# Kernel optimization log

Hardware: AMD Instinct MI355X
Metric: run time of the kernel (lower is better)

Reference implementation:

```python
import jax, jax.numpy as jnp
import numpy as np

H = 32  # hidden size (hard-coded in the torch module)

def _lstm_layer(x, W_ih, W_hh):
    # x: [B, T, F]; W_ih: [4H, F]; W_hh: [4H, H]; bias=False
    B = x.shape[0]
    # precompute input projection for all timesteps: [T, B, 4H]
    xg = jnp.einsum('btf,gf->tbg', x, W_ih)
    WhhT = W_hh.T  # [H, 4H]
    def step(carry, xg_t):
        h, c = carry
        gates = xg_t + h @ WhhT          # [B, 4H]
        i, f, g, o = jnp.split(gates, 4, axis=-1)  # PyTorch gate order i,f,g,o
        i = jax.nn.sigmoid(i)
        f = jax.nn.sigmoid(f)
        g = jnp.tanh(g)
        o = jax.nn.sigmoid(o)
        c = f * c + i * g
        h = o * jnp.tanh(c)
        return (h, c), h
    h0 = jnp.zeros((B, H), x.dtype)
    c0 = jnp.zeros((B, H), x.dtype)
    (hT, cT), hs = jax.lax.scan(step, (h0, c0), xg)
    return jnp.transpose(hs, (1, 0, 2)), hT, cT  # outputs [B,T,H], final h, final c


def setup_inputs() -> dict:
    key = jax.random.key(0)
    ks = jax.random.split(key, 8)
    B, T, F = 8192, 60, 158
    s_in = 1.0 / np.sqrt(H)  # PyTorch LSTM init scale
    inp = {
        'x':     jax.random.normal(ks[0], (B, T, F), jnp.float32),
        'W_ih0': jax.random.uniform(ks[1], (4 * H, F), jnp.float32, -s_in, s_in),
        'W_hh0': jax.random.uniform(ks[2], (4 * H, H), jnp.float32, -s_in, s_in),
        'W_ih1': jax.random.uniform(ks[3], (4 * H, H), jnp.float32, -s_in, s_in),
        'W_hh1': jax.random.uniform(ks[4], (4 * H, H), jnp.float32, -s_in, s_in),
        'W1':    jax.random.uniform(ks[5], (16, H), jnp.float32, -s_in, s_in),
        'b1':    jax.random.uniform(ks[6], (16,), jnp.float32, -s_in, s_in),
        'W2':    jax.random.uniform(ks[7], (1, 16), jnp.float32, -0.25, 0.25),
    }
    return inp


def reference(x, W_ih0, W_hh0, W_ih1, W_hh1, W1, b1, W2):
    out1, h1, c1 = _lstm_layer(x, W_ih0, W_hh0)      # layer 1 (inter-layer dropout inactive at eval)
    out2, h2, c2 = _lstm_layer(out1, W_ih1, W_hh1)   # layer 2
    # torch code: output, h_n = lstm(x) -> h_n is the TUPLE (h_n, c_n),
    # so h_n[-1] == c_n with shape [num_layers=2, B, H]
    c_n = jnp.stack([c1, c2], axis=0)                 # [2, B, H]
    y = jax.nn.relu(c_n @ W1.T + b1) @ W2.T           # [2, B, 1]
    return y
```

## Files before the change

### kernel.cpp

```cpp
#include <hip/hip_runtime.h>


constexpr int Bn = 8192, Tn = 60, Fn = 158, Hn = 32, Gn = 128;
constexpr int SKX = 168;
constexpr int SKH = 40;

typedef __attribute__((ext_vector_type(8))) short short8;
typedef __attribute__((ext_vector_type(4))) float floatx4;

__device__ __forceinline__ float sigm_(float x) {
    return __fdividef(1.f, 1.f + __expf(-x));
}
__device__ __forceinline__ float tanh_(float x) {
    return 1.f - __fdividef(2.f, __expf(2.f * x) + 1.f);
}
__device__ __forceinline__ unsigned short bf16r(float x) {
    unsigned u = __float_as_uint(x);
    return (unsigned short)((u + 0x7fffu + ((u >> 16) & 1u)) >> 16);
}
__device__ __forceinline__ float bf16f(unsigned short h) {
    return __uint_as_float(((unsigned)h) << 16);
}
__device__ __forceinline__ void cvt8(const float* v, short8& hi, short8& lo) {
#pragma unroll
    for (int j = 0; j < 8; ++j) {
        unsigned short h = bf16r(v[j]);
        hi[j] = (short)h;
        lo[j] = (short)bf16r(v[j] - bf16f(h));
    }
}

__global__ __launch_bounds__(256, 2) void lstm2_fused_kernel(
    const float* __restrict__ x,
    const float* __restrict__ Wih0, const float* __restrict__ Whh0,
    const float* __restrict__ Wih1, const float* __restrict__ Whh1,
    const float* __restrict__ W1, const float* __restrict__ b1,
    const float* __restrict__ W2, float* __restrict__ out) {
    __shared__ unsigned short sXh[2 * 16 * SKX];
    __shared__ unsigned short sXl[2 * 16 * SKX];
    __shared__ unsigned short sH1h[16 * SKH], sH1l[16 * SKH];
    __shared__ unsigned short sH2h[16 * SKH], sH2l[16 * SKH];
    __shared__ float sG[16 * 132];

    const int tid = threadIdx.x;
    const int wave = tid >> 6, lane = tid & 63;
    const int quad = lane >> 4, l15 = lane & 15;
    const int bBase = blockIdx.x * 16;

    short8 bX[5][2][2];
#pragma unroll
    for (int nt = 0; nt < 2; ++nt) {
        const int n = wave * 32 + nt * 16 + l15;
#pragma unroll
        for (int ks = 0; ks < 5; ++ks) {
            float wv[8];
#pragma unroll
            for (int j = 0; j < 8; ++j) {
                int k = ks * 32 + quad * 8 + j;
                wv[j] = (k < Fn) ? Wih0[n * Fn + k] : 0.f;
            }
            cvt8(wv, bX[ks][nt][0], bX[ks][nt][1]);
        }
    }
    short8 bW[3][2][2];
    const float* Wp[3] = {Whh0, Wih1, Whh1};
#pragma unroll
    for (int m = 0; m < 3; ++m)
#pragma unroll
        for (int nt = 0; nt < 2; ++nt) {
            const int n = wave * 32 + nt * 16 + l15;
            const float* wp = Wp[m] + n * Hn + quad * 8;
            float4 q0 = *(const float4*)(wp);
            float4 q1 = *(const float4*)(wp + 4);
            float wv[8] = {q0.x, q0.y, q0.z, q0.w, q1.x, q1.y, q1.z, q1.w};
            cvt8(wv, bW[m][nt][0], bW[m][nt][1]);
        }

    const float* xp[5];
    int soff[5];
    bool act[5];
#pragma unroll
    for (int r = 0; r < 5; ++r) {
        int i = tid + r * 256;
        act[r] = (i < 1264);
        int row = i / 79, c = i - row * 79;
        if (!act[r]) { row = 0; c = 0; }
        soff[r] = row * (SKX / 2) + c;
        xp[r] = x + (size_t)(bBase + row) * (Tn * Fn) + 2 * c;
    }
    auto stage = [&](const float2* v, int buf) {
        unsigned* dh = (unsigned*)sXh + buf * (16 * SKX / 2);
        unsigned* dl = (unsigned*)sXl + buf * (16 * SKX / 2);
#pragma unroll
        for (int r = 0; r < 5; ++r) {
            if (act[r]) {
                unsigned short h0 = bf16r(v[r].x), h1 = bf16r(v[r].y);
                unsigned short l0 = bf16r(v[r].x - bf16f(h0));
                unsigned short l1 = bf16r(v[r].y - bf16f(h1));
                dh[soff[r]] = (unsigned)h0 | ((unsigned)h1 << 16);
                dl[soff[r]] = (unsigned)l0 | ((unsigned)l1 << 16);
            }
        }
    };

    for (int i = tid; i < 320; i += 256) {
        ((unsigned*)sH1h)[i] = 0; ((unsigned*)sH1l)[i] = 0;
        ((unsigned*)sH2h)[i] = 0; ((unsigned*)sH2l)[i] = 0;
    }
    if (tid < 32) {
        int buf = tid >> 4, row = tid & 15;
        ((unsigned*)sXh)[buf * 1344 + row * 84 + 79] = 0;
        ((unsigned*)sXl)[buf * 1344 + row * 84 + 79] = 0;
    }

    {
        float2 v[5];
#pragma unroll
        for (int r = 0; r < 5; ++r) {
            v[r] = act[r] ? *(const float2*)xp[r] : make_float2(0.f, 0.f);
            xp[r] += Fn;
        }
        stage(v, 0);
    }

    const int aOffH = l15 * SKH + quad * 8;
    const int urow = tid >> 4, uj = (tid & 15) * 2;
    float c1x = 0.f, c1y = 0.f, c2x = 0.f, c2y = 0.f;
    __syncthreads();

    for (int t = 0; t < Tn; ++t) {
        const int buf = t & 1;
        float2 xr[5];
        if (t < Tn - 1) {
#pragma unroll
            for (int r = 0; r < 5; ++r) {
                xr[r] = act[r] ? *(const float2*)xp[r] : make_float2(0.f, 0.f);
                xp[r] += Fn;
            }
        }

        {
            const unsigned short* bxh = sXh + buf * (16 * SKX);
            const unsigned short* bxl = sXl + buf * (16 * SKX);
            short8 a1h = *(const short8*)(sH1h + aOffH);
            short8 a1l = *(const short8*)(sH1l + aOffH);
            floatx4 acc[2] = {};
#pragma unroll
            for (int ks = 0; ks < 5; ++ks) {
                const int off = l15 * SKX + ks * 32 + quad * 8;
                short8 xh = *(const short8*)(bxh + off);
                short8 xl = *(const short8*)(bxl + off);
#pragma unroll
                for (int nt = 0; nt < 2; ++nt) {
                    acc[nt] = __builtin_amdgcn_mfma_f32_16x16x32_bf16(xh, bX[ks][nt][0], acc[nt], 0, 0, 0);
                    acc[nt] = __builtin_amdgcn_mfma_f32_16x16x32_bf16(xh, bX[ks][nt][1], acc[nt], 0, 0, 0);
                    acc[nt] = __builtin_amdgcn_mfma_f32_16x16x32_bf16(xl, bX[ks][nt][0], acc[nt], 0, 0, 0);
                }
            }
#pragma unroll
            for (int nt = 0; nt < 2; ++nt) {
                acc[nt] = __builtin_amdgcn_mfma_f32_16x16x32_bf16(a1h, bW[0][nt][0], acc[nt], 0, 0, 0);
                acc[nt] = __builtin_amdgcn_mfma_f32_16x16x32_bf16(a1h, bW[0][nt][1], acc[nt], 0, 0, 0);
                acc[nt] = __builtin_amdgcn_mfma_f32_16x16x32_bf16(a1l, bW[0][nt][0], acc[nt], 0, 0, 0);
            }
#pragma unroll
            for (int nt = 0; nt < 2; ++nt)
#pragma unroll
                for (int reg = 0; reg < 4; ++reg)
                    sG[(quad * 4 + reg) * 132 + wave * 32 + nt * 16 + l15] = acc[nt][reg];
        }
        __syncthreads();

        {
            const float* g0 = sG + urow * 132 + uj;
            float2 ig = *(const float2*)(g0);
            float2 fg = *(const float2*)(g0 + 32);
            float2 gg = *(const float2*)(g0 + 64);
            float2 og = *(const float2*)(g0 + 96);
            c1x = sigm_(fg.x) * c1x + sigm_(ig.x) * tanh_(gg.x);
            c1y = sigm_(fg.y) * c1y + sigm_(ig.y) * tanh_(gg.y);
            float h0 = sigm_(og.x) * tanh_(c1x);
            float h1v = sigm_(og.y) * tanh_(c1y);
            unsigned short h0h = bf16r(h0), h1h = bf16r(h1v);
            unsigned short h0l = bf16r(h0 - bf16f(h0h)), h1l = bf16r(h1v - bf16f(h1h));
            *(unsigned*)(sH1h + urow * SKH + uj) = (unsigned)h0h | ((unsigned)h1h << 16);
            *(unsigned*)(sH1l + urow * SKH + uj) = (unsigned)h0l | ((unsigned)h1l << 16);
        }
        __syncthreads();

        {
            short8 a1h = *(const short8*)(sH1h + aOffH);
            short8 a1l = *(const short8*)(sH1l + aOffH);
            short8 a2h = *(const short8*)(sH2h + aOffH);
            short8 a2l = *(const short8*)(sH2l + aOffH);
            floatx4 acc[2] = {};
#pragma unroll
            for (int nt = 0; nt < 2; ++nt) {
                acc[nt] = __builtin_amdgcn_mfma_f32_16x16x32_bf16(a1h, bW[1][nt][0], acc[nt], 0, 0, 0);
                acc[nt] = __builtin_amdgcn_mfma_f32_16x16x32_bf16(a1h, bW[1][nt][1], acc[nt], 0, 0, 0);
                acc[nt] = __builtin_amdgcn_mfma_f32_16x16x32_bf16(a1l, bW[1][nt][0], acc[nt], 0, 0, 0);
                acc[nt] = __builtin_amdgcn_mfma_f32_16x16x32_bf16(a2h, bW[2][nt][0], acc[nt], 0, 0, 0);
                acc[nt] = __builtin_amdgcn_mfma_f32_16x16x32_bf16(a2h, bW[2][nt][1], acc[nt], 0, 0, 0);
                acc[nt] = __builtin_amdgcn_mfma_f32_16x16x32_bf16(a2l, bW[2][nt][0], acc[nt], 0, 0, 0);
            }
#pragma unroll
            for (int nt = 0; nt < 2; ++nt)
#pragma unroll
                for (int reg = 0; reg < 4; ++reg)
                    sG[(quad * 4 + reg) * 132 + wave * 32 + nt * 16 + l15] = acc[nt][reg];
        }
        if (t < Tn - 1) stage(xr, buf ^ 1);
        __syncthreads();

        {
            const float* g0 = sG + urow * 132 + uj;
            float2 ig = *(const float2*)(g0);
            float2 fg = *(const float2*)(g0 + 32);
            float2 gg = *(const float2*)(g0 + 64);
            float2 og = *(const float2*)(g0 + 96);
            c2x = sigm_(fg.x) * c2x + sigm_(ig.x) * tanh_(gg.x);
            c2y = sigm_(fg.y) * c2y + sigm_(ig.y) * tanh_(gg.y);
            float h0 = sigm_(og.x) * tanh_(c2x);
            float h1v = sigm_(og.y) * tanh_(c2y);
            unsigned short h0h = bf16r(h0), h1h = bf16r(h1v);
            unsigned short h0l = bf16r(h0 - bf16f(h0h)), h1l = bf16r(h1v - bf16f(h1h));
            *(unsigned*)(sH2h + urow * SKH + uj) = (unsigned)h0h | ((unsigned)h1h << 16);
            *(unsigned*)(sH2l + urow * SKH + uj) = (unsigned)h0l | ((unsigned)h1l << 16);
        }
        __syncthreads();
    }

    float* sC = sG;
    *(float2*)(sC + urow * 33 + uj) = make_float2(c1x, c1y);
    *(float2*)(sC + 528 + urow * 33 + uj) = make_float2(c2x, c2y);
    __syncthreads();
    if (tid < 32) {
        int l = tid >> 4, b = tid & 15;
        const float* cc = sC + l * 528 + b * 33;
        float y = 0.f;
#pragma unroll 1
        for (int q = 0; q < 16; ++q) {
            float s = b1[q];
#pragma unroll
            for (int j = 0; j < 32; ++j) s = fmaf(cc[j], W1[q * 32 + j], s);
            y = fmaf(fmaxf(s, 0.f), W2[q], y);
        }
        out[l * Bn + bBase + b] = y;
    }
}

extern "C" void kernel_launch(void* const* d_in, const int* in_sizes, int n_in,
                              void* d_out, int out_size, void* d_ws, size_t ws_size,
                              hipStream_t stream) {
    const float* x    = (const float*)d_in[0];
    const float* Wih0 = (const float*)d_in[1];
    const float* Whh0 = (const float*)d_in[2];
    const float* Wih1 = (const float*)d_in[3];
    const float* Whh1 = (const float*)d_in[4];
    const float* W1   = (const float*)d_in[5];
    const float* b1   = (const float*)d_in[6];
    const float* W2   = (const float*)d_in[7];
    float* out = (float*)d_out;

    lstm2_fused_kernel<<<Bn / 16, 256, 0, stream>>>(x, Wih0, Whh0, Wih1, Whh1,
                                                    W1, b1, W2, out);
}
```

Measured before the change: 489.4 us.

## Skew LSTM layers across timesteps, switch to fp16 split with scaled residual

```diff
diff --git a/kernel.cpp b/kernel.cpp
--- a/kernel.cpp
+++ b/kernel.cpp
@@ -1,11 +1,15 @@
 #include <hip/hip_runtime.h>
 
 
-constexpr int Bn = 8192, Tn = 60, Fn = 158, Hn = 32, Gn = 128;
+constexpr int Bn = 8192, Tn = 60, Fn = 158, Hn = 32;
 constexpr int SKX = 168;
 constexpr int SKH = 40;
-
-typedef __attribute__((ext_vector_type(8))) short short8;
+constexpr int SG = 132;
+constexpr float LS = 4096.f;
+constexpr float ILS = 1.f / 4096.f;
+
+typedef _Float16 half8 __attribute__((ext_vector_type(8)));
+typedef __fp16 half2f __attribute__((ext_vector_type(2)));
 typedef __attribute__((ext_vector_type(4))) float floatx4;
 
 __device__ __forceinline__ float sigm_(float x) {
@@ -14,19 +18,18 @@
 __device__ __forceinline__ float tanh_(float x) {
     return 1.f - __fdividef(2.f, __expf(2.f * x) + 1.f);
 }
-__device__ __forceinline__ unsigned short bf16r(float x) {
-    unsigned u = __float_as_uint(x);
-    return (unsigned short)((u + 0x7fffu + ((u >> 16) & 1u)) >> 16);
-}
-__device__ __forceinline__ float bf16f(unsigned short h) {
-    return __uint_as_float(((unsigned)h) << 16);
-}
-__device__ __forceinline__ void cvt8(const float* v, short8& hi, short8& lo) {
-#pragma unroll
-    for (int j = 0; j < 8; ++j) {
-        unsigned short h = bf16r(v[j]);
-        hi[j] = (short)h;
-        lo[j] = (short)bf16r(v[j] - bf16f(h));
+__device__ __forceinline__ unsigned h2u(half2f h) {
+    return __builtin_bit_cast(unsigned, h);
+}
+__device__ __forceinline__ void cvt8h(const float* v, half8& hi, half8& lo) {
+#pragma unroll
+    for (int j = 0; j < 8; j += 2) {
+        half2f h = __builtin_amdgcn_cvt_pkrtz(v[j], v[j + 1]);
+        float r0 = (v[j] - (float)h[0]) * LS;
+        float r1 = (v[j + 1] - (float)h[1]) * LS;
+        half2f l = __builtin_amdgcn_cvt_pkrtz(r0, r1);
+        hi[j] = (_Float16)h[0]; hi[j + 1] = (_Float16)h[1];
+        lo[j] = (_Float16)l[0]; lo[j + 1] = (_Float16)l[1];
     }
 }
 
@@ -40,14 +43,15 @@
     __shared__ unsigned short sXl[2 * 16 * SKX];
     __shared__ unsigned short sH1h[16 * SKH], sH1l[16 * SKH];
     __shared__ unsigned short sH2h[16 * SKH], sH2l[16 * SKH];
-    __shared__ float sG[16 * 132];
+    __shared__ float sG1[16 * SG];
+    __shared__ float sG2[16 * SG];
 
     const int tid = threadIdx.x;
     const int wave = tid >> 6, lane = tid & 63;
     const int quad = lane >> 4, l15 = lane & 15;
     const int bBase = blockIdx.x * 16;
 
-    short8 bX[5][2][2];
+    half8 bX[5][2][2];
 #pragma unroll
     for (int nt = 0; nt < 2; ++nt) {
         const int n = wave * 32 + nt * 16 + l15;
@@ -59,10 +63,10 @@
                 int k = ks * 32 + quad * 8 + j;
                 wv[j] = (k < Fn) ? Wih0[n * Fn + k] : 0.f;
             }
-            cvt8(wv, bX[ks][nt][0], bX[ks][nt][1]);
-        }
-    }
-    short8 bW[3][2][2];
+            cvt8h(wv, bX[ks][nt][0], bX[ks][nt][1]);
+        }
+    }
+    half8 bW[3][2][2];
     const float* Wp[3] = {Whh0, Wih1, Whh1};
 #pragma unroll
     for (int m = 0; m < 3; ++m)
@@ -73,7 +77,7 @@
             float4 q0 = *(const float4*)(wp);
             float4 q1 = *(const float4*)(wp + 4);
             float wv[8] = {q0.x, q0.y, q0.z, q0.w, q1.x, q1.y, q1.z, q1.w};
-            cvt8(wv, bW[m][nt][0], bW[m][nt][1]);
+            cvt8h(wv, bW[m][nt][0], bW[m][nt][1]);
         }
 
     const float* xp[5];
@@ -94,11 +98,11 @@
 #pragma unroll
         for (int r = 0; r < 5; ++r) {
             if (act[r]) {
-                unsigned short h0 = bf16r(v[r].x), h1 = bf16r(v[r].y);
-                unsigned short l0 = bf16r(v[r].x - bf16f(h0));
-                unsigned short l1 = bf16r(v[r].y - bf16f(h1));
-                dh[soff[r]] = (unsigned)h0 | ((unsigned)h1 << 16);
-                dl[soff[r]] = (unsigned)l0 | ((unsigned)l1 << 16);
+                half2f h = __builtin_amdgcn_cvt_pkrtz(v[r].x, v[r].y);
+                half2f l = __builtin_amdgcn_cvt_pkrtz(
+                    (v[r].x - (float)h[0]) * LS, (v[r].y - (float)h[1]) * LS);
+                dh[soff[r]] = h2u(h);
+                dl[soff[r]] = h2u(l);
             }
         }
     };
@@ -113,126 +117,156 @@
         ((unsigned*)sXl)[buf * 1344 + row * 84 + 79] = 0;
     }
 
-    {
+#pragma unroll
+    for (int t0 = 0; t0 < 2; ++t0) {
         float2 v[5];
 #pragma unroll
         for (int r = 0; r < 5; ++r) {
             v[r] = act[r] ? *(const float2*)xp[r] : make_float2(0.f, 0.f);
             xp[r] += Fn;
         }
-        stage(v, 0);
+        stage(v, t0);
     }
 
     const int aOffH = l15 * SKH + quad * 8;
-    const int urow = tid >> 4, uj = (tid & 15) * 2;
+    const int urow = tid >> 4, hp = (tid & 15) * 2;
     float c1x = 0.f, c1y = 0.f, c2x = 0.f, c2y = 0.f;
-    __syncthreads();
-
-    for (int t = 0; t < Tn; ++t) {
-        const int buf = t & 1;
+
+    auto upd = [&](const float* sGx, unsigned short* sHh, unsigned short* sHl,
+                   float& cx, float& cy) {
+        const float* g = sGx + urow * SG + hp * 4;
+        float4 A = *(const float4*)g;
+        float4 Bv = *(const float4*)(g + 4);
+        cx = sigm_(A.y) * cx + sigm_(A.x) * tanh_(A.z);
+        cy = sigm_(Bv.y) * cy + sigm_(Bv.x) * tanh_(Bv.z);
+        float h0 = sigm_(A.w) * tanh_(cx);
+        float h1v = sigm_(Bv.w) * tanh_(cy);
+        half2f hh = __builtin_amdgcn_cvt_pkrtz(h0, h1v);
+        half2f hl = __builtin_amdgcn_cvt_pkrtz((h0 - (float)hh[0]) * LS,
+                                               (h1v - (float)hh[1]) * LS);
+        *(unsigned*)(sHh + urow * SKH + hp) = h2u(hh);
+        *(unsigned*)(sHl + urow * SKH + hp) = h2u(hl);
+    };
+
+    __syncthreads();
+
+    {
+        floatx4 aH[2] = {}, aL[2] = {};
+#pragma unroll
+        for (int ks = 0; ks < 5; ++ks) {
+            const int off = l15 * SKX + ks * 32 + quad * 8;
+            half8 xh = *(const half8*)(sXh + off);
+            half8 xl = *(const half8*)(sXl + off);
+#pragma unroll
+            for (int nt = 0; nt < 2; ++nt) {
+                aH[nt] = __builtin_amdgcn_mfma_f32_16x16x32_f16(xh, bX[ks][nt][0], aH[nt], 0, 0, 0);
+                aL[nt] = __builtin_amdgcn_mfma_f32_16x16x32_f16(xh, bX[ks][nt][1], aL[nt], 0, 0, 0);
+                aL[nt] = __builtin_amdgcn_mfma_f32_16x16x32_f16(xl, bX[ks][nt][0], aL[nt], 0, 0, 0);
+            }
+        }
+#pragma unroll
+        for (int nt = 0; nt < 2; ++nt)
+#pragma unroll
+            for (int reg = 0; reg < 4; ++reg)
+                sG1[(quad * 4 + reg) * SG + (nt * 16 + l15) * 4 + wave] =
+                    fmaf(ILS, aL[nt][reg], aH[nt][reg]);
+    }
+    __syncthreads();
+    upd(sG1, sH1h, sH1l, c1x, c1y);
+    __syncthreads();
+
+    for (int i = 0; i < Tn - 1; ++i) {
         float2 xr[5];
-        if (t < Tn - 1) {
+        const bool pf = (i + 2 < Tn);
+        if (pf) {
 #pragma unroll
             for (int r = 0; r < 5; ++r) {
                 xr[r] = act[r] ? *(const float2*)xp[r] : make_float2(0.f, 0.f);
                 xp[r] += Fn;
             }
         }
-
         {
-            const unsigned short* bxh = sXh + buf * (16 * SKX);
-            const unsigned short* bxl = sXl + buf * (16 * SKX);
-            short8 a1h = *(const short8*)(sH1h + aOffH);
-            short8 a1l = *(const short8*)(sH1l + aOffH);
-            floatx4 acc[2] = {};
+            const unsigned short* bxh = sXh + ((i + 1) & 1) * (16 * SKX);
+            const unsigned short* bxl = sXl + ((i + 1) & 1) * (16 * SKX);
+            half8 a1h = *(const half8*)(sH1h + aOffH);
+            half8 a1l = *(const half8*)(sH1l + aOffH);
+            half8 a2h = *(const half8*)(sH2h + aOffH);
+            half8 a2l = *(const half8*)(sH2l + aOffH);
+            floatx4 a1H[2] = {}, a1L[2] = {}, a2H[2] = {}, a2L[2] = {};
 #pragma unroll
             for (int ks = 0; ks < 5; ++ks) {
                 const int off = l15 * SKX + ks * 32 + quad * 8;
-                short8 xh = *(const short8*)(bxh + off);
-                short8 xl = *(const short8*)(bxl + off);
+                half8 xh = *(const half8*)(bxh + off);
+                half8 xl = *(const half8*)(bxl + off);
 #pragma unroll
                 for (int nt = 0; nt < 2; ++nt) {
-                    acc[nt] = __builtin_amdgcn_mfma_f32_16x16x32_bf16(xh, bX[ks][nt][0], acc[nt], 0, 0, 0);
-                    acc[nt] = __builtin_amdgcn_mfma_f32_16x16x32_bf16(xh, bX[ks][nt][1], acc[nt], 0, 0, 0);
-                    acc[nt] = __builtin_amdgcn_mfma_f32_16x16x32_bf16(xl, bX[ks][nt][0], acc[nt], 0, 0, 0);
+                    a1H[nt] = __builtin_amdgcn_mfma_f32_16x16x32_f16(xh, bX[ks][nt][0], a1H[nt], 0, 0, 0);
+                    a1L[nt] = __builtin_amdgcn_mfma_f32_16x16x32_f16(xh, bX[ks][nt][1], a1L[nt], 0, 0, 0);
+                    a1L[nt] = __builtin_amdgcn_mfma_f32_16x16x32_f16(xl, bX[ks][nt][0], a1L[nt], 0, 0, 0);
                 }
             }
 #pragma unroll
             for (int nt = 0; nt < 2; ++nt) {
-                acc[nt] = __builtin_amdgcn_mfma_f32_16x16x32_bf16(a1h, bW[0][nt][0], acc[nt], 0, 0, 0);
-                acc[nt] = __builtin_amdgcn_mfma_f32_16x16x32_bf16(a1h, bW[0][nt][1], acc[nt], 0, 0, 0);
-                acc[nt] = __builtin_amdgcn_mfma_f32_16x16x32_bf16(a1l, bW[0][nt][0], acc[nt], 0, 0, 0);
+                a1H[nt] = __builtin_amdgcn_mfma_f32_16x16x32_f16(a1h, bW[0][nt][0], a1H[nt], 0, 0, 0);
+                a1L[nt] = __builtin_amdgcn_mfma_f32_16x16x32_f16(a1h, bW[0][nt][1], a1L[nt], 0, 0, 0);
+                a1L[nt] = __builtin_amdgcn_mfma_f32_16x16x32_f16(a1l, bW[0][nt][0], a1L[nt], 0, 0, 0);
+                a2H[nt] = __builtin_amdgcn_mfma_f32_16x16x32_f16(a1h, bW[1][nt][0], a2H[nt], 0, 0, 0);
+                a2L[nt] = __builtin_amdgcn_mfma_f32_16x16x32_f16(a1h, bW[1][nt][1], a2L[nt], 0, 0, 0);
+                a2L[nt] = __builtin_amdgcn_mfma_f32_16x16x32_f16(a1l, bW[1][nt][0], a2L[nt], 0, 0, 0);
+                a2H[nt] = __builtin_amdgcn_mfma_f32_16x16x32_f16(a2h, bW[2][nt][0], a2H[nt], 0, 0, 0);
+                a2L[nt] = __builtin_amdgcn_mfma_f32_16x16x32_f16(a2h, bW[2][nt][1], a2L[nt], 0, 0, 0);
+                a2L[nt] = __builtin_amdgcn_mfma_f32_16x16x32_f16(a2l, bW[2][nt][0], a2L[nt], 0, 0, 0);
             }
 #pragma unroll
             for (int nt = 0; nt < 2; ++nt)
 #pragma unroll
-                for (int reg = 0; reg < 4; ++reg)
-                    sG[(quad * 4 + reg) * 132 + wave * 32 + nt * 16 + l15] = acc[nt][reg];
-        }
+                for (int reg = 0; reg < 4; ++reg) {
+                    const int idx = (quad * 4 + reg) * SG + (nt * 16 + l15) * 4 + wave;
+                    sG1[idx] = fmaf(ILS, a1L[nt][reg], a1H[nt][reg]);
+                    sG2[idx] = fmaf(ILS, a2L[nt][reg], a2H[nt][reg]);
+                }
+        }
+        if (pf) stage(xr, i & 1);
         __syncthreads();
-
-        {
-            const float* g0 = sG + urow * 132 + uj;
-            float2 ig = *(const float2*)(g0);
-            float2 fg = *(const float2*)(g0 + 32);
-            float2 gg = *(const float2*)(g0 + 64);
-            float2 og = *(const float2*)(g0 + 96);
-            c1x = sigm_(fg.x) * c1x + sigm_(ig.x) * tanh_(gg.x);
-            c1y = sigm_(fg.y) * c1y + sigm_(ig.y) * tanh_(gg.y);
-            float h0 = sigm_(og.x) * tanh_(c1x);
-            float h1v = sigm_(og.y) * tanh_(c1y);
-            unsigned short h0h = bf16r(h0), h1h = bf16r(h1v);
-            unsigned short h0l = bf16r(h0 - bf16f(h0h)), h1l = bf16r(h1v - bf16f(h1h));
-            *(unsigned*)(sH1h + urow * SKH + uj) = (unsigned)h0h | ((unsigned)h1h << 16);
-            *(unsigned*)(sH1l + urow * SKH + uj) = (unsigned)h0l | ((unsigned)h1l << 16);
-        }
+        upd(sG2, sH2h, sH2l, c2x, c2y);
+        upd(sG1, sH1h, sH1l, c1x, c1y);
         __syncthreads();
-
-        {
-            short8 a1h = *(const short8*)(sH1h + aOffH);
-            short8 a1l = *(const short8*)(sH1l + aOffH);
-            short8 a2h = *(const short8*)(sH2h + aOffH);
-            short8 a2l = *(const short8*)(sH2l + aOffH);
-            floatx4 acc[2] = {};
-#pragma unroll
-            for (int nt = 0; nt < 2; ++nt) {
-                acc[nt] = __builtin_amdgcn_mfma_f32_16x16x32_bf16(a1h, bW[1][nt][0], acc[nt], 0, 0, 0);
-                acc[nt] = __builtin_amdgcn_mfma_f32_16x16x32_bf16(a1h, bW[1][nt][1], acc[nt], 0, 0, 0);
-                acc[nt] = __builtin_amdgcn_mfma_f32_16x16x32_bf16(a1l, bW[1][nt][0], acc[nt], 0, 0, 0);
-                acc[nt] = __builtin_amdgcn_mfma_f32_16x16x32_bf16(a2h, bW[2][nt][0], acc[nt], 0, 0, 0);
-                acc[nt] = __builtin_amdgcn_mfma_f32_16x16x32_bf16(a2h, bW[2][nt][1], acc[nt], 0, 0, 0);
-                acc[nt] = __builtin_amdgcn_mfma_f32_16x16x32_bf16(a2l, bW[2][nt][0], acc[nt], 0, 0, 0);
-            }
-#pragma unroll
-            for (int nt = 0; nt < 2; ++nt)
-#pragma unroll
-                for (int reg = 0; reg < 4; ++reg)
-                    sG[(quad * 4 + reg) * 132 + wave * 32 + nt * 16 + l15] = acc[nt][reg];
-        }
-        if (t < Tn - 1) stage(xr, buf ^ 1);
-        __syncthreads();
-
-        {
-            const float* g0 = sG + urow * 132 + uj;
-            float2 ig = *(const float2*)(g0);
-            float2 fg = *(const float2*)(g0 + 32);
-            float2 gg = *(const float2*)(g0 + 64);
-            float2 og = *(const float2*)(g0 + 96);
-            c2x = sigm_(fg.x) * c2x + sigm_(ig.x) * tanh_(gg.x);
-            c2y = sigm_(fg.y) * c2y + sigm_(ig.y) * tanh_(gg.y);
-            float h0 = sigm_(og.x) * tanh_(c2x);
-            float h1v = sigm_(og.y) * tanh_(c2y);
-            unsigned short h0h = bf16r(h0), h1h = bf16r(h1v);
-            unsigned short h0l = bf16r(h0 - bf16f(h0h)), h1l = bf16r(h1v - bf16f(h1h));
-            *(unsigned*)(sH2h + urow * SKH + uj) = (unsigned)h0h | ((unsigned)h1h << 16);
-            *(unsigned*)(sH2l + urow * SKH + uj) = (unsigned)h0l | ((unsigned)h1l << 16);
-        }
-        __syncthreads();
-    }
-
-    float* sC = sG;
-    *(float2*)(sC + urow * 33 + uj) = make_float2(c1x, c1y);
-    *(float2*)(sC + 528 + urow * 33 + uj) = make_float2(c2x, c2y);
+    }
+
+    {
+        half8 a1h = *(const half8*)(sH1h + aOffH);
+        half8 a1l = *(const half8*)(sH1l + aOffH);
+        half8 a2h = *(const half8*)(sH2h + aOffH);
+        half8 a2l = *(const half8*)(sH2l + aOffH);
+        floatx4 aH[2] = {}, aL[2] = {};
+#pragma unroll
+        for (int nt = 0; nt < 2; ++nt) {
+            aH[nt] = __builtin_amdgcn_mfma_f32_16x16x32_f16(a1h, bW[1][nt][0], aH[nt], 0, 0, 0);
+            aL[nt] = __builtin_amdgcn_mfma_f32_16x16x32_f16(a1h, bW[1][nt][1], aL[nt], 0, 0, 0);
+            aL[nt] = __builtin_amdgcn_mfma_f32_16x16x32_f16(a1l, bW[1][nt][0], aL[nt], 0, 0, 0);
+            aH[nt] = __builtin_amdgcn_mfma_f32_16x16x32_f16(a2h, bW[2][nt][0], aH[nt], 0, 0, 0);
+            aL[nt] = __builtin_amdgcn_mfma_f32_16x16x32_f16(a2h, bW[2][nt][1], aL[nt], 0, 0, 0);
+            aL[nt] = __builtin_amdgcn_mfma_f32_16x16x32_f16(a2l, bW[2][nt][0], aL[nt], 0, 0, 0);
+        }
+#pragma unroll
+        for (int nt = 0; nt < 2; ++nt)
+#pragma unroll
+            for (int reg = 0; reg < 4; ++reg)
+                sG2[(quad * 4 + reg) * SG + (nt * 16 + l15) * 4 + wave] =
+                    fmaf(ILS, aL[nt][reg], aH[nt][reg]);
+    }
+    __syncthreads();
+    {
+        const float* g = sG2 + urow * SG + hp * 4;
+        float4 A = *(const float4*)g;
+        float4 Bv = *(const float4*)(g + 4);
+        c2x = sigm_(A.y) * c2x + sigm_(A.x) * tanh_(A.z);
+        c2y = sigm_(Bv.y) * c2y + sigm_(Bv.x) * tanh_(Bv.z);
+    }
+
+    float* sC = sG1;
+    *(float2*)(sC + urow * 33 + hp) = make_float2(c1x, c1y);
+    *(float2*)(sC + 528 + urow * 33 + hp) = make_float2(c2x, c2y);
     __syncthreads();
     if (tid < 32) {
         int l = tid >> 4, b = tid & 15;
```

New measurement: 473.6 us. 1.03x faster.
